# Kernel optimization log

Hardware: AMD Instinct MI355X
Metric: run time of the kernel (lower is better)

The kernel has to match this reference:

```python
import jax, jax.numpy as jnp
import numpy as np

U, I, E, D, R = 100000, 50000, 2000000, 64, 5


def setup_inputs() -> dict:
    key = jax.random.key(0)
    ks = jax.random.split(key, 14)
    def n(k, shape, scale=0.05):
        return jax.random.normal(k, shape, jnp.float32) * scale
    return {
        "user_feat": n(ks[0], (U, D), 1.0),
        "item_feat": n(ks[1], (I, D), 1.0),
        "rating_feat": n(ks[2], (R, D), 1.0),
        "row_idxs": jax.random.randint(ks[3], (E,), 0, I),   # item index per edge
        "col_idxs": jax.random.randint(ks[4], (E,), 0, U),   # user index per edge (dst)
        "rating": jax.random.randint(ks[5], (E,), 0, R),
        # gv = Linear(2D,D)+ReLU -> Linear(D,D)+ReLU
        "gv_w1": n(ks[6], (2 * D, D)), "gv_b1": jnp.zeros((D,), jnp.float32),
        "gv_w2": n(ks[7], (D, D)),     "gv_b2": jnp.zeros((D,), jnp.float32),
        # Attention: Linear(2D,D)+ReLU -> Linear(D,D)+ReLU -> Linear(D,1)
        "att_w1": n(ks[8], (2 * D, D)), "att_b1": jnp.zeros((D,), jnp.float32),
        "att_w2": n(ks[9], (D, D)),     "att_b2": jnp.zeros((D,), jnp.float32),
        "att_w3": n(ks[10], (D, 1)),    "att_b3": jnp.zeros((1,), jnp.float32),
        # output projection w = Linear(D,D)
        "w_w": n(ks[11], (D, D)), "w_b": jnp.zeros((D,), jnp.float32),
    }


def segment_softmax(logits, seg, num_segments):
    # numerically stable softmax over edges grouped by destination node
    m = jax.ops.segment_max(logits, seg, num_segments=num_segments)
    e = jnp.exp(logits - m[seg])
    s = jax.ops.segment_sum(e, seg, num_segments=num_segments)
    return e / s[seg]


def reference(user_feat, item_feat, rating_feat, row_idxs, col_idxs, rating,
              gv_w1, gv_b1, gv_w2, gv_b2,
              att_w1, att_b1, att_w2, att_b2, att_w3, att_b3,
              w_w, w_b):
    # gather per-edge embeddings
    r_emb = rating_feat[rating]          # [E, D]
    i_emb = item_feat[row_idxs]          # [E, D]
    u_emb = user_feat[col_idxs]          # [E, D]
    # gv MLP on concat(item, rating)
    x = jnp.concatenate([i_emb, r_emb], axis=1)              # [E, 2D]
    h1 = jax.nn.relu(x @ gv_w1 + gv_b1)
    x_ia = jax.nn.relu(h1 @ gv_w2 + gv_b2)                   # [E, D]
    # attention MLP on concat(x_ia, user)
    a = jnp.concatenate([x_ia, u_emb], axis=1)               # [E, 2D]
    a = jax.nn.relu(a @ att_w1 + att_b1)
    a = jax.nn.relu(a @ att_w2 + att_b2)
    weight = (a @ att_w3 + att_b3)[:, 0]                     # [E]
    # edge_softmax over incoming edges of each destination (user) node
    value = segment_softmax(weight, col_idxs, U)             # [E]
    # scatter-sum weighted messages to users
    h = jax.ops.segment_sum(x_ia * value[:, None], col_idxs, num_segments=U)  # [U, D]
    # act is None -> plain linear
    return h @ w_w + w_b
```

## Files before the change

kernel.cpp:

```cpp
#include <hip/hip_runtime.h>
#include <hip/hip_bf16.h>

#define U_N 100000
#define I_N 50000
#define E_N 2000000
#define R_N 5
#define C_N (I_N*R_N)
#define NBLK_U 391
#define NBLK_E 7813
#define NBLK_C 1954
#define NBUCKC 196

typedef __hip_bfloat16 bf16_t;
typedef unsigned short u16;
typedef unsigned char u8;
typedef __attribute__((ext_vector_type(8))) short bf16x8;
typedef __attribute__((ext_vector_type(4))) float f32x4;

__device__ __forceinline__ float blo(unsigned u){ return __uint_as_float(u<<16); }
__device__ __forceinline__ float bhi(unsigned u){ return __uint_as_float(u & 0xffff0000u); }
__device__ __forceinline__ unsigned pkbf(float a, float b){
  __hip_bfloat162 t = __float22bfloat162_rn(float2{a,b});
  union { __hip_bfloat162 h; unsigned u; } cv; cv.h = t; return cv.u;
}
__device__ __forceinline__ u16 f2b(float v){
  union { __hip_bfloat16 h; u16 u; } cv; cv.h = __float2bfloat16(v); return cv.u;
}
__device__ __forceinline__ unsigned relu_add_pk(unsigned a, unsigned b){
  return pkbf(fmaxf(blo(a)+blo(b),0.f), fmaxf(bhi(a)+bhi(b),0.f));
}

__global__ __launch_bounds__(256) void k_histQ(const int* __restrict__ cols, int* __restrict__ hist_g){
  __shared__ int histI[NBUCKC];
  int t = threadIdx.x, b = blockIdx.x;
  if(t < NBUCKC) histI[t] = 0;
  __syncthreads();
  int e = b*256 + t;
  if(e < E_N) atomicAdd(&histI[cols[e] >> 9], 1);
  __syncthreads();
  if(t < NBUCKC) hist_g[(size_t)b*NBUCKC + t] = histI[t];
}

__global__ __launch_bounds__(256) void k_scanQ(const int* __restrict__ hist_g, int* __restrict__ boff_g,
                                               int* __restrict__ qtot){
  __shared__ int wsum[4];
  int t = threadIdx.x, q = blockIdx.x;
  int lane = t & 63, wv = t >> 6;
  int running = 0;
  for(int c0=0; c0<NBLK_E; c0+=256){
    int b = c0 + t;
    int v = (b < NBLK_E) ? hist_g[(size_t)b*NBUCKC + q] : 0;
    int inc = v;
#pragma unroll
    for(int off=1; off<64; off<<=1){
      int x = __shfl(inc, lane-off);
      if(lane >= off) inc += x;
    }
    if(lane == 63) wsum[wv] = inc;
    __syncthreads();
    int w0=wsum[0], w1=wsum[1], w2=wsum[2], w3=wsum[3];
    int wpre = (wv>0?w0:0) + (wv>1?w1:0) + (wv>2?w2:0);
    if(b < NBLK_E) boff_g[(size_t)b*NBUCKC + q] = running + wpre + inc - v;
    running += w0 + w1 + w2 + w3;
    __syncthreads();
  }
  if(t == 0) qtot[q] = running;
}

__global__ void k_scanT(const int* __restrict__ qtot, int* __restrict__ qbase){
  __shared__ int s[256];
  int t = threadIdx.x;
  int v = (t < NBUCKC) ? qtot[t] : 0;
  s[t] = v; __syncthreads();
  for(int off=1; off<256; off<<=1){
    int x = (t>=off) ? s[t-off] : 0;
    __syncthreads();
    s[t] += x;
    __syncthreads();
  }
  if(t < NBUCKC) qbase[t] = s[t] - v;
  if(t == 255)   qbase[NBUCKC] = s[255];
}

__global__ __launch_bounds__(256) void k_place2(const int* __restrict__ rows, const int* __restrict__ cols,
                                                const int* __restrict__ rats,
                                                const int* __restrict__ boff_g, const int* __restrict__ qbase,
                                                unsigned* __restrict__ uc2){
  __shared__ int rankI[NBUCKC];
  __shared__ int baseI[NBUCKC];
  int t = threadIdx.x, b = blockIdx.x;
  if(t < NBUCKC){
    rankI[t] = 0;
    baseI[t] = qbase[t] + boff_g[(size_t)b*NBUCKC + t];
  }
  __syncthreads();
  int e = b*256 + t;
  if(e < E_N){
    int u = cols[e];
    int c = rows[e]*5 + rats[e];
    int q = u >> 9;
    int r = atomicAdd(&rankI[q], 1);
    uc2[baseI[q] + r] = ((unsigned)(u & 511) << 18) | (unsigned)c;
  }
}

__global__ __launch_bounds__(256) void k_fineB1(const unsigned* __restrict__ uc2, const int* __restrict__ qbase,
                                                int* __restrict__ cnt){
  __shared__ int hist[512];
  int t = threadIdx.x, q = blockIdx.x;
  hist[t] = 0; hist[t+256] = 0;
  __syncthreads();
  int r0 = qbase[q], r1 = qbase[q+1];
  for(int j=r0+t; j<r1; j+=256) atomicAdd(&hist[(uc2[j]>>18) & 511], 1);
  __syncthreads();
  cnt[q*512 + t]       = hist[t];
  cnt[q*512 + t + 256] = hist[t+256];
}

__global__ __launch_bounds__(256) void k_scanA(const int* __restrict__ cnt, int* __restrict__ start,
                                               int* __restrict__ bsum){
  __shared__ int s[256];
  int t = threadIdx.x, i = blockIdx.x*256 + t;
  int v = (i < U_N) ? cnt[i] : 0;
  s[t] = v; __syncthreads();
  for(int off=1; off<256; off<<=1){
    int x = (t>=off) ? s[t-off] : 0;
    __syncthreads();
    s[t] += x;
    __syncthreads();
  }
  start[i] = s[t] - v;
  if(t == 255) bsum[blockIdx.x] = s[255];
}

__global__ void k_scanB(int* bsum, int n){
  __shared__ int s[512];
  int t = threadIdx.x;
  int v = (t < n) ? bsum[t] : 0;
  s[t] = v; __syncthreads();
  for(int off=1; off<512; off<<=1){
    int x = (t>=off) ? s[t-off] : 0;
    __syncthreads();
    s[t] += x;
    __syncthreads();
  }
  if(t < n) bsum[t] = s[t] - v;
}

__global__ __launch_bounds__(256) void k_scanC(int* start, const int* __restrict__ bsum){
  int i = blockIdx.x*256 + threadIdx.x;
  start[i] += bsum[blockIdx.x];
}

__global__ __launch_bounds__(256) void k_fineB2(const unsigned* __restrict__ uc2, const int* __restrict__ qbase,
                                                const int* __restrict__ start,
                                                int* __restrict__ u_s, int* __restrict__ c_s){
  __shared__ int fillb[512];
  __shared__ int startb[512];
  int t = threadIdx.x, q = blockIdx.x;
  fillb[t] = 0; fillb[t+256] = 0;
  startb[t]     = start[q*512 + t];
  startb[t+256] = start[q*512 + t + 256];
  __syncthreads();
  int r0 = qbase[q], r1 = qbase[q+1];
  for(int j=r0+t; j<r1; j+=256){
    unsigned v = uc2[j];
    int ul = (int)((v>>18) & 511);
    int off = atomicAdd(&fillb[ul], 1);
    int pos = startb[ul] + off;
    u_s[pos] = (q<<9) | ul;
    c_s[pos] = (int)(v & 0x3FFFFu);
  }
}

__global__ void k_ratpart(const float* __restrict__ rf, const float* __restrict__ w1,
                          const float* __restrict__ b1, float* __restrict__ out){
  int t = threadIdx.x; if(t >= R_N*64) return;
  int r = t>>6, d = t&63;
  float acc = b1[d];
  for(int k=0;k<64;k++) acc += rf[r*64 + k] * w1[(64+k)*64 + d];
  out[t] = acc;
}

__global__ __launch_bounds__(256) void k_prepw6(const float* __restrict__ w1, const float* __restrict__ a1,
                                                const float* __restrict__ w2, const float* __restrict__ a2,
                                                const float* __restrict__ ww,
                                                u16* w1t, u16* u1t, u16* w2t, u16* a1t, u16* a2t, u16* wwt){
  int idx = (blockIdx.x & 15)*256 + threadIdx.x;
  int sec = blockIdx.x >> 4;
  int d = idx >> 6, k = idx & 63;
  const float* src; u16* dst; int ko = 0;
  switch(sec){
    case 0: src=w1; dst=w1t; break;
    case 1: src=a1; dst=u1t; ko=64; break;
    case 2: src=w2; dst=w2t; break;
    case 3: src=a1; dst=a1t; break;
    case 4: src=a2; dst=a2t; break;
    default: src=ww; dst=wwt; break;
  }
  dst[idx] = f2b(src[(size_t)(ko+k)*64 + d]);
}

template<bool BIAS>
__global__ __launch_bounds__(256) void k_rowgemm(const float4* __restrict__ in,
                                                 const uint4* __restrict__ wt,
                                                 const float* __restrict__ bias,
                                                 uint4* __restrict__ outp, int n){
  __shared__ uint4 A_u4[2048];
  __shared__ uint4 W_u4[512];
  __shared__ float bsh[64];
  u16* A16 = (u16*)A_u4;
  const int tid = threadIdx.x;
  for(int cid = tid; cid < 512; cid += 256){
    int dd = cid >> 3, ch = cid & 7;
    W_u4[dd*8 + (ch ^ (dd&7))] = wt[cid];
  }
  if(BIAS && tid < 64) bsh[tid] = bias[tid];
  const int base = blockIdx.x*256;
  const int ch = tid & 7;
#pragma unroll
  for(int it=0; it<8; ++it){
    int s = it*32 + (tid>>3);
    int r = base + s;
    uint4 o = {0,0,0,0};
    if(r < n){
      const float4* p = in + (size_t)r*16 + ch*2;
      float4 v0 = p[0], v1 = p[1];
      o.x = pkbf(v0.x, v0.y); o.y = pkbf(v0.z, v0.w);
      o.z = pkbf(v1.x, v1.y); o.w = pkbf(v1.z, v1.w);
    }
    A_u4[s*8 + (ch ^ (s&7))] = o;
  }
  __syncthreads();
  const int l = tid & 63, w = tid >> 6;
  const int lr = l & 15, g = l >> 4;
  bf16x8 bfr[4][2];
#pragma unroll
  for(int nt=0; nt<4; ++nt)
#pragma unroll
    for(int kk=0; kk<2; ++kk){
      int d = nt*16 + lr;
      bfr[nt][kk] = *(const bf16x8*)&W_u4[d*8 + ((kk*4+g) ^ (d&7))];
    }
  float bv[4];
#pragma unroll
  for(int nt=0; nt<4; ++nt) bv[nt] = BIAS ? bsh[nt*16 + lr] : 0.f;
#pragma unroll
  for(int t=0; t<4; ++t){
    int s = w*64 + t*16 + lr;
    bf16x8 af0 = *(const bf16x8*)&A_u4[s*8 + ((0*4+g) ^ (s&7))];
    bf16x8 af1 = *(const bf16x8*)&A_u4[s*8 + ((1*4+g) ^ (s&7))];
    f32x4 acc[4];
#pragma unroll
    for(int nt=0; nt<4; ++nt){
      f32x4 c0 = { bv[nt], bv[nt], bv[nt], bv[nt] };
      c0 = __builtin_amdgcn_mfma_f32_16x16x32_bf16(af0, bfr[nt][0], c0, 0, 0, 0);
      c0 = __builtin_amdgcn_mfma_f32_16x16x32_bf16(af1, bfr[nt][1], c0, 0, 0, 0);
      acc[nt] = c0;
    }
#pragma unroll
    for(int nt=0; nt<4; ++nt){
      int d = nt*16 + lr;
#pragma unroll
      for(int reg=0; reg<4; ++reg){
        int srow = w*64 + t*16 + g*4 + reg;
        A16[srow*64 + ((d>>3)^(srow&7))*8 + (d&7)] = f2b(acc[nt][reg]);
      }
    }
  }
#pragma unroll
  for(int it=0; it<8; ++it){
    int s = w*64 + it*8 + (l>>3);
    int c2 = l & 7;
    int r = base + s;
    if(r < n) outp[(size_t)r*8 + c2] = A_u4[s*8 + (c2 ^ (s&7))];
  }
}

__global__ __launch_bounds__(256) void k_combo_mfma(const uint4* __restrict__ itemp,
                                                    const float4* __restrict__ ratp,
                                                    const uint4* __restrict__ w2t_g, const uint4* __restrict__ a1t_g,
                                                    const uint4* __restrict__ wwt_g,
                                                    const float* __restrict__ b2,
                                                    uint4* __restrict__ y_o, uint4* __restrict__ xa1_o){
  __shared__ uint4 A_u4[1024];
  __shared__ uint4 X_u4[1024];
  __shared__ uint4 W2_u4[512];
  __shared__ uint4 A1_u4[512];
  __shared__ uint4 WW_u4[512];
  __shared__ float4 rsh4[80];
  __shared__ float b2sh[64];
  u16* A16 = (u16*)A_u4;
  u16* X16 = (u16*)X_u4;
  const int tid = threadIdx.x;
  for(int cid = tid; cid < 512; cid += 256){
    int dd = cid >> 3, ch = cid & 7;
    W2_u4[dd*8 + (ch ^ (dd&7))] = w2t_g[cid];
    A1_u4[dd*8 + (ch ^ (dd&7))] = a1t_g[cid];
    WW_u4[dd*8 + (ch ^ (dd&7))] = wwt_g[cid];
  }
  if(tid < 80) rsh4[tid] = ratp[tid];
  if(tid < 64) b2sh[tid] = b2[tid];
  __syncthreads();

  const int base = blockIdx.x*128;
  const int ch = tid & 7;
#pragma unroll
  for(int it=0; it<4; ++it){
    int s = it*32 + (tid>>3);
    int cidx = base + s;
    uint4 o = {0,0,0,0};
    if(cidx < C_N){
      int i = cidx/5, r = cidx - i*5;
      uint4 iv = itemp[(size_t)i*8 + ch];
      float4 r0 = rsh4[r*16 + ch*2], r1 = rsh4[r*16 + ch*2 + 1];
      o.x = pkbf(fmaxf(blo(iv.x)+r0.x,0.f), fmaxf(bhi(iv.x)+r0.y,0.f));
      o.y = pkbf(fmaxf(blo(iv.y)+r0.z,0.f), fmaxf(bhi(iv.y)+r0.w,0.f));
      o.z = pkbf(fmaxf(blo(iv.z)+r1.x,0.f), fmaxf(bhi(iv.z)+r1.y,0.f));
      o.w = pkbf(fmaxf(blo(iv.w)+r1.z,0.f), fmaxf(bhi(iv.w)+r1.w,0.f));
    }
    A_u4[s*8 + (ch ^ (s&7))] = o;
  }
  __syncthreads();

  const int l = tid & 63, w = tid >> 6;
  const int lr = l & 15, g = l >> 4;
  bf16x8 w2f[4][2], a1f[4][2], wwf[4][2];
#pragma unroll
  for(int nt=0; nt<4; ++nt)
#pragma unroll
    for(int kk=0; kk<2; ++kk){
      int d = nt*16 + lr;
      w2f[nt][kk] = *(const bf16x8*)&W2_u4[d*8 + ((kk*4+g) ^ (d&7))];
      a1f[nt][kk] = *(const bf16x8*)&A1_u4[d*8 + ((kk*4+g) ^ (d&7))];
      wwf[nt][kk] = *(const bf16x8*)&WW_u4[d*8 + ((kk*4+g) ^ (d&7))];
    }
  float b2v[4];
#pragma unroll
  for(int nt=0; nt<4; ++nt) b2v[nt] = b2sh[nt*16 + lr];

#pragma unroll
  for(int t=0; t<2; ++t){
    int s = w*32 + t*16 + lr;
    bf16x8 af0 = *(const bf16x8*)&A_u4[s*8 + ((0*4+g) ^ (s&7))];
    bf16x8 af1 = *(const bf16x8*)&A_u4[s*8 + ((1*4+g) ^ (s&7))];
#pragma unroll
    for(int nt=0; nt<4; ++nt){
      f32x4 c0 = { b2v[nt], b2v[nt], b2v[nt], b2v[nt] };
      c0 = __builtin_amdgcn_mfma_f32_16x16x32_bf16(af0, w2f[nt][0], c0, 0, 0, 0);
      c0 = __builtin_amdgcn_mfma_f32_16x16x32_bf16(af1, w2f[nt][1], c0, 0, 0, 0);
      int d = nt*16 + lr;
#pragma unroll
      for(int reg=0; reg<4; ++reg){
        int srow = w*32 + t*16 + g*4 + reg;
        X16[srow*64 + ((d>>3)^(srow&7))*8 + (d&7)] = f2b(fmaxf(c0[reg], 0.f));
      }
    }
    bf16x8 xf0 = *(const bf16x8*)&X_u4[s*8 + ((0*4+g) ^ (s&7))];
    bf16x8 xf1 = *(const bf16x8*)&X_u4[s*8 + ((1*4+g) ^ (s&7))];
#pragma unroll
    for(int nt=0; nt<4; ++nt){
      f32x4 c0 = { 0.f, 0.f, 0.f, 0.f };
      c0 = __builtin_amdgcn_mfma_f32_16x16x32_bf16(xf0, a1f[nt][0], c0, 0, 0, 0);
      c0 = __builtin_amdgcn_mfma_f32_16x16x32_bf16(xf1, a1f[nt][1], c0, 0, 0, 0);
      int d = nt*16 + lr;
#pragma unroll
      for(int reg=0; reg<4; ++reg){
        int srow = w*32 + t*16 + g*4 + reg;
        A16[srow*64 + ((d>>3)^(srow&7))*8 + (d&7)] = f2b(c0[reg]);
      }
    }
#pragma unroll
    for(int nt=0; nt<4; ++nt){
      f32x4 c0 = { 0.f, 0.f, 0.f, 0.f };
      c0 = __builtin_amdgcn_mfma_f32_16x16x32_bf16(xf0, wwf[nt][0], c0, 0, 0, 0);
      c0 = __builtin_amdgcn_mfma_f32_16x16x32_bf16(xf1, wwf[nt][1], c0, 0, 0, 0);
      int d = nt*16 + lr;
#pragma unroll
      for(int reg=0; reg<4; ++reg){
        int srow = w*32 + t*16 + g*4 + reg;
        X16[srow*64 + ((d>>3)^(srow&7))*8 + (d&7)] = f2b(c0[reg]);
      }
    }
  }
#pragma unroll
  for(int it=0; it<4; ++it){
    int s = w*32 + it*8 + (l>>3);
    int c2 = l & 7;
    int r = base + s;
    if(r < C_N){
      y_o  [(size_t)r*8 + c2] = X_u4[s*8 + (c2 ^ (s&7))];
      xa1_o[(size_t)r*8 + c2] = A_u4[s*8 + (c2 ^ (s&7))];
    }
  }
}

__global__ __launch_bounds__(256) void k_edge_mfma(const int* __restrict__ u_s, const int* __restrict__ c_s,
                                                   const uint4* __restrict__ xa1p, const uint4* __restrict__ userp,
                                                   const u16* __restrict__ w2t_g,
                                                   const float* __restrict__ a2b,
                                                   const float* __restrict__ a3w, const float* __restrict__ a3b,
                                                   float* __restrict__ wlog){
  const int tid = threadIdx.x;
  const int base = blockIdx.x*256;
  const int l = tid & 63, w = tid >> 6;
  const int lr = l & 15;
  const int g  = l >> 4;
  bf16x8 bf[4][2];
#pragma unroll
  for(int nt=0; nt<4; ++nt)
#pragma unroll
    for(int kk=0; kk<2; ++kk){
      int d = nt*16 + lr;
      bf[nt][kk] = *(const bf16x8*)(w2t_g + d*64 + kk*32 + g*8);
    }
  float b2v[4], a3v[4];
#pragma unroll
  for(int nt=0; nt<4; ++nt){ b2v[nt] = a2b[nt*16 + lr]; a3v[nt] = a3w[nt*16 + lr]; }
  const float a3b0 = a3b[0];

  int cin[4], uin[4];
#pragma unroll
  for(int t=0; t<4; ++t){
    int s = base + w*64 + t*16 + lr;
    cin[t] = (s < E_N) ? c_s[s] : 0;
    uin[t] = (s < E_N) ? u_s[s] : 0;
  }
  uint4 xv0 = xa1p[(size_t)cin[0]*8 + g];
  uint4 uv0 = userp[(size_t)uin[0]*8 + g];
  uint4 xv1 = xa1p[(size_t)cin[0]*8 + 4 + g];
  uint4 uv1 = userp[(size_t)uin[0]*8 + 4 + g];

#pragma unroll
  for(int t=0; t<4; ++t){
    uint4 nx0, nu0, nx1, nu1;
    if(t < 3){
      nx0 = xa1p[(size_t)cin[t+1]*8 + g];
      nu0 = userp[(size_t)uin[t+1]*8 + g];
      nx1 = xa1p[(size_t)cin[t+1]*8 + 4 + g];
      nu1 = userp[(size_t)uin[t+1]*8 + 4 + g];
    }
    union { uint4 u4; bf16x8 v; } a0, a1;
    a0.u4.x = relu_add_pk(xv0.x, uv0.x);
    a0.u4.y = relu_add_pk(xv0.y, uv0.y);
    a0.u4.z = relu_add_pk(xv0.z, uv0.z);
    a0.u4.w = relu_add_pk(xv0.w, uv0.w);
    a1.u4.x = relu_add_pk(xv1.x, uv1.x);
    a1.u4.y = relu_add_pk(xv1.y, uv1.y);
    a1.u4.z = relu_add_pk(xv1.z, uv1.z);
    a1.u4.w = relu_add_pk(xv1.w, uv1.w);
    f32x4 acc[4];
#pragma unroll
    for(int nt=0; nt<4; ++nt){
      f32x4 c0 = { b2v[nt], b2v[nt], b2v[nt], b2v[nt] };
      c0 = __builtin_amdgcn_mfma_f32_16x16x32_bf16(a0.v, bf[nt][0], c0, 0, 0, 0);
      c0 = __builtin_amdgcn_mfma_f32_16x16x32_bf16(a1.v, bf[nt][1], c0, 0, 0, 0);
      acc[nt] = c0;
    }
    float s0=0.f, s1=0.f, s2=0.f, s3=0.f;
#pragma unroll
    for(int nt=0; nt<4; ++nt){
      s0 += fmaxf(acc[nt][0], 0.f) * a3v[nt];
      s1 += fmaxf(acc[nt][1], 0.f) * a3v[nt];
      s2 += fmaxf(acc[nt][2], 0.f) * a3v[nt];
      s3 += fmaxf(acc[nt][3], 0.f) * a3v[nt];
    }
#pragma unroll
    for(int mask=1; mask<16; mask<<=1){
      s0 += __shfl_xor(s0, mask);
      s1 += __shfl_xor(s1, mask);
      s2 += __shfl_xor(s2, mask);
      s3 += __shfl_xor(s3, mask);
    }
    if(lr == 0){
      int e0 = base + w*64 + t*16 + g*4;
      if(e0+0 < E_N) wlog[e0+0] = s0 + a3b0;
      if(e0+1 < E_N) wlog[e0+1] = s1 + a3b0;
      if(e0+2 < E_N) wlog[e0+2] = s2 + a3b0;
      if(e0+3 < E_N) wlog[e0+3] = s3 + a3b0;
    }
    xv0 = nx0; uv0 = nu0; xv1 = nx1; uv1 = nu1;
  }
}

__global__ __launch_bounds__(256) void k_smax(const int* __restrict__ start,
                                              const float* __restrict__ wlog,
                                              u16* __restrict__ pval){
  int w = threadIdx.x >> 6, lane = threadIdx.x & 63;
  int u = blockIdx.x*4 + w;
  int s0 = start[u], n = start[u+1] - s0;
  int nq = (n + 63) >> 6;
  float tq[4];
  float m = -1e30f;
  for(int q=0; q<nq; ++q){
    int j = q*64 + lane;
    float t = (j<n) ? wlog[s0+j] : -1e30f;
    if(q<4) tq[q] = t;
    m = fmaxf(m, t);
  }
#pragma unroll
  for(int off=32; off>=1; off>>=1) m = fmaxf(m, __shfl_xor(m, off));
  float ssum = 0.f;
  for(int q=0; q<nq; ++q){
    int j = q*64 + lane;
    float t = (q<4) ? tq[q] : ((j<n) ? wlog[s0+j] : -1e30f);
    float e = (j<n) ? __expf(t - m) : 0.f;
    if(q<4) tq[q] = e;
    ssum += e;
  }
#pragma unroll
  for(int off=32; off>=1; off>>=1) ssum += __shfl_xor(ssum, off);
  float inv = (n>0) ? (1.f/ssum) : 0.f;
  for(int q=0; q<nq; ++q){
    int j = q*64 + lane;
    float e = (q<4) ? tq[q] : ((j<n) ? __expf(wlog[s0+j] - m) : 0.f);
    if(j<n) pval[s0+j] = f2b(e * inv);
  }
}

__global__ __launch_bounds__(256) void k_agg(const int* __restrict__ start,
                                             const int* __restrict__ u_s, const int* __restrict__ c_s,
                                             const u16* __restrict__ pval,
                                             const u16* __restrict__ Y,
                                             const float* __restrict__ wb,
                                             float* __restrict__ out){
  __shared__ uint4 Ysh[4][256];
  int w = threadIdx.x >> 6, l = threadIdx.x & 63;
  int lr = l & 15, g = l >> 4;
  int base = (blockIdx.x*4 + w) * 16;
  if(base >= U_N) return;
  int s0g = start[base];
  int s1g = start[base+16];
  int myu = base + lr;
  float wbv[4];
#pragma unroll
  for(int nt=0; nt<4; ++nt) wbv[nt] = wb[nt*16 + lr];
  f32x4 acc[4];
#pragma unroll
  for(int nt=0; nt<4; ++nt) acc[nt] = f32x4{ wbv[nt], wbv[nt], wbv[nt], wbv[nt] };

  u16* Ysh16 = (u16*)&Ysh[w][0];
  const int kb = g*8;
  int sA = s0g & ~31;
  int nch = (s1g - sA + 31) >> 5;
  for(int ch=0; ch<nch; ++ch){
    int e0 = sA + ch*32;
    int rowe = e0 + (l>>1);
    int crow = c_s[rowe];
    const uint4* yp = (const uint4*)Y + (size_t)crow*8 + (l&1)*4;
    uint4* dst = &Ysh[w][(l>>1)*8 + (l&1)*4];
    dst[0] = yp[0]; dst[1] = yp[1]; dst[2] = yp[2]; dst[3] = yp[3];

    bf16x8 pv = *(const bf16x8*)(pval + e0 + kb);
    int4 u0 = *(const int4*)(u_s + e0 + kb);
    int4 u1 = *(const int4*)(u_s + e0 + kb + 4);
    bf16x8 af;
    af[0] = (u0.x == myu) ? pv[0] : (short)0;
    af[1] = (u0.y == myu) ? pv[1] : (short)0;
    af[2] = (u0.z == myu) ? pv[2] : (short)0;
    af[3] = (u0.w == myu) ? pv[3] : (short)0;
    af[4] = (u1.x == myu) ? pv[4] : (short)0;
    af[5] = (u1.y == myu) ? pv[5] : (short)0;
    af[6] = (u1.z == myu) ? pv[6] : (short)0;
    af[7] = (u1.w == myu) ? pv[7] : (short)0;
    bf16x8 b0, b1, b2, b3;
#pragma unroll
    for(int j=0; j<8; ++j){
      int r = (kb + j)*64 + lr;
      b0[j] = (short)Ysh16[r];
      b1[j] = (short)Ysh16[r+16];
      b2[j] = (short)Ysh16[r+32];
      b3[j] = (short)Ysh16[r+48];
    }
    acc[0] = __builtin_amdgcn_mfma_f32_16x16x32_bf16(af, b0, acc[0], 0, 0, 0);
    acc[1] = __builtin_amdgcn_mfma_f32_16x16x32_bf16(af, b1, acc[1], 0, 0, 0);
    acc[2] = __builtin_amdgcn_mfma_f32_16x16x32_bf16(af, b2, acc[2], 0, 0, 0);
    acc[3] = __builtin_amdgcn_mfma_f32_16x16x32_bf16(af, b3, acc[3], 0, 0, 0);
  }
#pragma unroll
  for(int nt=0; nt<4; ++nt){
#pragma unroll
    for(int reg=0; reg<4; ++reg){
      int u = base + g*4 + reg;
      out[(size_t)u*64 + nt*16 + lr] = acc[nt][reg];
    }
  }
}

extern "C" void kernel_launch(void* const* d_in, const int* in_sizes, int n_in,
                              void* d_out, int out_size, void* d_ws, size_t ws_size,
                              hipStream_t stream){
  (void)in_sizes; (void)n_in; (void)out_size; (void)ws_size;
  const float4* user_feat  = (const float4*)d_in[0];
  const float4* item_feat  = (const float4*)d_in[1];
  const float*  rating_feat= (const float*)d_in[2];
  const int*    rows       = (const int*)d_in[3];
  const int*    cols       = (const int*)d_in[4];
  const int*    rats       = (const int*)d_in[5];
  const float* gv_w1 = (const float*)d_in[6];
  const float* gv_b1 = (const float*)d_in[7];
  const float* gv_w2 = (const float*)d_in[8];
  const float* gv_b2 = (const float*)d_in[9];
  const float* att_w1= (const float*)d_in[10];
  const float* att_b1= (const float*)d_in[11];
  const float* att_w2= (const float*)d_in[12];
  const float* att_b2= (const float*)d_in[13];
  const float* att_w3= (const float*)d_in[14];
  const float* att_b3= (const float*)d_in[15];
  const float* w_w   = (const float*)d_in[16];
  const float* w_b   = (const float*)d_in[17];
  float* out = (float*)d_out;

  char* ws = (char*)d_ws; size_t off = 0;
  auto take = [&](size_t b)->char*{ char* p = ws + off; off = (off + b + 255) & ~(size_t)255; return p; };
  bf16_t*   item_part  = (bf16_t*)take((size_t)I_N*64*2);
  bf16_t*   user_part  = (bf16_t*)take((size_t)U_N*64*2);
  float*    rating_part= (float*) take((size_t)R_N*64*4);
  bf16_t*   y_t        = (bf16_t*)take((size_t)C_N*64*2);
  bf16_t*   xa1_t      = (bf16_t*)take((size_t)C_N*64*2);
  float*    wlog_s     = (float*) take((size_t)E_N*4);
  int*      c_s        = (int*)   take((size_t)E_N*4);
  int*      u_s        = (int*)   take((size_t)E_N*4);
  u16*      pval       = (u16*)   take((size_t)E_N*2);
  unsigned* uc2        = (unsigned*)take((size_t)E_N*4);
  int*      hist_g     = (int*)   take((size_t)NBLK_E*NBUCKC*4);
  int*      boff_g     = (int*)   take((size_t)NBLK_E*NBUCKC*4);
  int*      qtot       = (int*)   take((size_t)256*4);
  int*      qbase      = (int*)   take((size_t)256*4);
  int*      cnt        = (int*)   take((size_t)(NBUCKC*512+256)*4);
  int*      start      = (int*)   take((size_t)(NBUCKC*512+256)*4);
  int*      bsum       = (int*)   take((size_t)512*4);
  u16*      w1t        = (u16*)   take((size_t)4096*2);
  u16*      u1t        = (u16*)   take((size_t)4096*2);
  u16*      w2t        = (u16*)   take((size_t)4096*2);
  u16*      a1t        = (u16*)   take((size_t)4096*2);
  u16*      a2t        = (u16*)   take((size_t)4096*2);
  u16*      wwt        = (u16*)   take((size_t)4096*2);

  k_histQ <<<NBLK_E, 256, 0, stream>>>(cols, hist_g);
  k_scanQ <<<NBUCKC, 256, 0, stream>>>(hist_g, boff_g, qtot);
  k_scanT <<<1, 256, 0, stream>>>(qtot, qbase);
  k_place2<<<NBLK_E, 256, 0, stream>>>(rows, cols, rats, boff_g, qbase, uc2);
  k_fineB1<<<NBUCKC, 256, 0, stream>>>(uc2, qbase, cnt);
  k_scanA <<<NBLK_U, 256, 0, stream>>>(cnt, start, bsum);
  k_scanB <<<1, 512, 0, stream>>>(bsum, NBLK_U);
  k_scanC <<<NBLK_U, 256, 0, stream>>>(start, bsum);
  k_fineB2<<<NBUCKC, 256, 0, stream>>>(uc2, qbase, start, u_s, c_s);
  k_ratpart <<<1, 320, 0, stream>>>(rating_feat, gv_w1, gv_b1, rating_part);
  k_prepw6  <<<96, 256, 0, stream>>>(gv_w1, att_w1, gv_w2, att_w2, w_w, w1t, u1t, w2t, a1t, a2t, wwt);
  k_rowgemm<false><<<(I_N+255)/256, 256, 0, stream>>>(item_feat, (const uint4*)w1t, nullptr,
                                                      (uint4*)item_part, I_N);
  k_rowgemm<true> <<<NBLK_U, 256, 0, stream>>>(user_feat, (const uint4*)u1t, att_b1,
                                               (uint4*)user_part, U_N);
  k_combo_mfma<<<NBLK_C, 256, 0, stream>>>((const uint4*)item_part, (const float4*)rating_part,
                                           (const uint4*)w2t, (const uint4*)a1t, (const uint4*)wwt, gv_b2,
                                           (uint4*)y_t, (uint4*)xa1_t);
  k_edge_mfma<<<NBLK_E, 256, 0, stream>>>(u_s, c_s, (const uint4*)xa1_t, (const uint4*)user_part,
                                          w2t, att_b2, att_w3, att_b3, wlog_s);
  k_smax <<<U_N/4, 256, 0, stream>>>(start, wlog_s, pval);
  k_agg  <<<(U_N/64)+1, 256, 0, stream>>>(start, u_s, c_s, pval, (const u16*)y_t, w_b, out);
}
```

Measured before the change: 329.5 us.

## Store xa1 table in FP8 and fuse segment softmax into aggregation kernel

The per-(item,rating) attention pre-activation table is now written as FP8 e4m3 instead of bf16, which halves the bytes each edge gathers in the edge MLP kernel. The separate softmax kernel and its bf16 probability array are removed. The aggregation kernel now computes the per-user max in a first pass over the edges, then exponentiates inside the MFMA accumulation loop and normalizes by the sum at the end. This saves a kernel launch and a round trip of per-edge values, but reads the logits and user ids twice and loses precision from the FP8 storage.

```diff
diff --git a/kernel.cpp b/kernel.cpp
--- a/kernel.cpp
+++ b/kernel.cpp
@@ -1,5 +1,6 @@
 #include <hip/hip_runtime.h>
 #include <hip/hip_bf16.h>
+#include <hip/hip_fp8.h>
 
 #define U_N 100000
 #define I_N 50000
@@ -26,8 +27,11 @@
 __device__ __forceinline__ u16 f2b(float v){
   union { __hip_bfloat16 h; u16 u; } cv; cv.h = __float2bfloat16(v); return cv.u;
 }
-__device__ __forceinline__ unsigned relu_add_pk(unsigned a, unsigned b){
-  return pkbf(fmaxf(blo(a)+blo(b),0.f), fmaxf(bhi(a)+bhi(b),0.f));
+__device__ __forceinline__ float f8f(unsigned b){
+  __hip_fp8_e4m3 h; h.__x = (u8)b; return (float)h;
+}
+__device__ __forceinline__ unsigned ff8(float f){
+  __hip_fp8_e4m3 h(f); return (unsigned)h.__x;
 }
 
 __global__ __launch_bounds__(256) void k_histQ(const int* __restrict__ cols, int* __restrict__ hist_g){
@@ -282,7 +286,7 @@
                                                     const uint4* __restrict__ w2t_g, const uint4* __restrict__ a1t_g,
                                                     const uint4* __restrict__ wwt_g,
                                                     const float* __restrict__ b2,
-                                                    uint4* __restrict__ y_o, uint4* __restrict__ xa1_o){
+                                                    uint4* __restrict__ y_o, u8* __restrict__ xa1_o8){
   __shared__ uint4 A_u4[1024];
   __shared__ uint4 X_u4[1024];
   __shared__ uint4 W2_u4[512];
@@ -388,15 +392,30 @@
     int s = w*32 + it*8 + (l>>3);
     int c2 = l & 7;
     int r = base + s;
+    if(r < C_N) y_o[(size_t)r*8 + c2] = X_u4[s*8 + (c2 ^ (s&7))];
+  }
+#pragma unroll
+  for(int it=0; it<2; ++it){
+    int slot = it*64 + l;
+    int rl = slot >> 2;
+    int c4 = slot & 3;
+    int s = w*32 + rl;
+    int r = base + s;
     if(r < C_N){
-      y_o  [(size_t)r*8 + c2] = X_u4[s*8 + (c2 ^ (s&7))];
-      xa1_o[(size_t)r*8 + c2] = A_u4[s*8 + (c2 ^ (s&7))];
+      uint4 h0 = A_u4[s*8 + ((c4*2+0) ^ (s&7))];
+      uint4 h1 = A_u4[s*8 + ((c4*2+1) ^ (s&7))];
+      uint4 o;
+      o.x = ff8(blo(h0.x)) | (ff8(bhi(h0.x))<<8) | (ff8(blo(h0.y))<<16) | (ff8(bhi(h0.y))<<24);
+      o.y = ff8(blo(h0.z)) | (ff8(bhi(h0.z))<<8) | (ff8(blo(h0.w))<<16) | (ff8(bhi(h0.w))<<24);
+      o.z = ff8(blo(h1.x)) | (ff8(bhi(h1.x))<<8) | (ff8(blo(h1.y))<<16) | (ff8(bhi(h1.y))<<24);
+      o.w = ff8(blo(h1.z)) | (ff8(bhi(h1.z))<<8) | (ff8(blo(h1.w))<<16) | (ff8(bhi(h1.w))<<24);
+      *(uint4*)(xa1_o8 + (size_t)r*64 + c4*16) = o;
     }
   }
 }
 
 __global__ __launch_bounds__(256) void k_edge_mfma(const int* __restrict__ u_s, const int* __restrict__ c_s,
-                                                   const uint4* __restrict__ xa1p, const uint4* __restrict__ userp,
+                                                   const u8* __restrict__ xa1p8, const uint4* __restrict__ userp,
                                                    const u16* __restrict__ w2t_g,
                                                    const float* __restrict__ a2b,
                                                    const float* __restrict__ a3w, const float* __restrict__ a3b,
@@ -426,29 +445,29 @@
     cin[t] = (s < E_N) ? c_s[s] : 0;
     uin[t] = (s < E_N) ? u_s[s] : 0;
   }
-  uint4 xv0 = xa1p[(size_t)cin[0]*8 + g];
+  uint2 xq0 = *(const uint2*)(xa1p8 + (size_t)cin[0]*64 + g*8);
+  uint2 xq1 = *(const uint2*)(xa1p8 + (size_t)cin[0]*64 + 32 + g*8);
   uint4 uv0 = userp[(size_t)uin[0]*8 + g];
-  uint4 xv1 = xa1p[(size_t)cin[0]*8 + 4 + g];
   uint4 uv1 = userp[(size_t)uin[0]*8 + 4 + g];
 
 #pragma unroll
   for(int t=0; t<4; ++t){
-    uint4 nx0, nu0, nx1, nu1;
+    uint2 nx0, nx1; uint4 nu0, nu1;
     if(t < 3){
-      nx0 = xa1p[(size_t)cin[t+1]*8 + g];
+      nx0 = *(const uint2*)(xa1p8 + (size_t)cin[t+1]*64 + g*8);
+      nx1 = *(const uint2*)(xa1p8 + (size_t)cin[t+1]*64 + 32 + g*8);
       nu0 = userp[(size_t)uin[t+1]*8 + g];
-      nx1 = xa1p[(size_t)cin[t+1]*8 + 4 + g];
       nu1 = userp[(size_t)uin[t+1]*8 + 4 + g];
     }
     union { uint4 u4; bf16x8 v; } a0, a1;
-    a0.u4.x = relu_add_pk(xv0.x, uv0.x);
-    a0.u4.y = relu_add_pk(xv0.y, uv0.y);
-    a0.u4.z = relu_add_pk(xv0.z, uv0.z);
-    a0.u4.w = relu_add_pk(xv0.w, uv0.w);
-    a1.u4.x = relu_add_pk(xv1.x, uv1.x);
-    a1.u4.y = relu_add_pk(xv1.y, uv1.y);
-    a1.u4.z = relu_add_pk(xv1.z, uv1.z);
-    a1.u4.w = relu_add_pk(xv1.w, uv1.w);
+    a0.u4.x = pkbf(fmaxf(f8f(xq0.x&255u)+blo(uv0.x),0.f),       fmaxf(f8f((xq0.x>>8)&255u)+bhi(uv0.x),0.f));
+    a0.u4.y = pkbf(fmaxf(f8f((xq0.x>>16)&255u)+blo(uv0.y),0.f), fmaxf(f8f(xq0.x>>24)+bhi(uv0.y),0.f));
+    a0.u4.z = pkbf(fmaxf(f8f(xq0.y&255u)+blo(uv0.z),0.f),       fmaxf(f8f((xq0.y>>8)&255u)+bhi(uv0.z),0.f));
+    a0.u4.w = pkbf(fmaxf(f8f((xq0.y>>16)&255u)+blo(uv0.w),0.f), fmaxf(f8f(xq0.y>>24)+bhi(uv0.w),0.f));
+    a1.u4.x = pkbf(fmaxf(f8f(xq1.x&255u)+blo(uv1.x),0.f),       fmaxf(f8f((xq1.x>>8)&255u)+bhi(uv1.x),0.f));
+    a1.u4.y = pkbf(fmaxf(f8f((xq1.x>>16)&255u)+blo(uv1.y),0.f), fmaxf(f8f(xq1.x>>24)+bhi(uv1.y),0.f));
+    a1.u4.z = pkbf(fmaxf(f8f(xq1.y&255u)+blo(uv1.z),0.f),       fmaxf(f8f((xq1.y>>8)&255u)+bhi(uv1.z),0.f));
+    a1.u4.w = pkbf(fmaxf(f8f((xq1.y>>16)&255u)+blo(uv1.w),0.f), fmaxf(f8f(xq1.y>>24)+bhi(uv1.w),0.f));
     f32x4 acc[4];
 #pragma unroll
     for(int nt=0; nt<4; ++nt){
@@ -479,51 +498,16 @@
       if(e0+2 < E_N) wlog[e0+2] = s2 + a3b0;
       if(e0+3 < E_N) wlog[e0+3] = s3 + a3b0;
     }
-    xv0 = nx0; uv0 = nu0; xv1 = nx1; uv1 = nu1;
-  }
-}
-
-__global__ __launch_bounds__(256) void k_smax(const int* __restrict__ start,
+    xq0 = nx0; xq1 = nx1; uv0 = nu0; uv1 = nu1;
+  }
+}
+
+__global__ __launch_bounds__(256) void k_aggf(const int* __restrict__ start,
+                                              const int* __restrict__ u_s, const int* __restrict__ c_s,
                                               const float* __restrict__ wlog,
-                                              u16* __restrict__ pval){
-  int w = threadIdx.x >> 6, lane = threadIdx.x & 63;
-  int u = blockIdx.x*4 + w;
-  int s0 = start[u], n = start[u+1] - s0;
-  int nq = (n + 63) >> 6;
-  float tq[4];
-  float m = -1e30f;
-  for(int q=0; q<nq; ++q){
-    int j = q*64 + lane;
-    float t = (j<n) ? wlog[s0+j] : -1e30f;
-    if(q<4) tq[q] = t;
-    m = fmaxf(m, t);
-  }
-#pragma unroll
-  for(int off=32; off>=1; off>>=1) m = fmaxf(m, __shfl_xor(m, off));
-  float ssum = 0.f;
-  for(int q=0; q<nq; ++q){
-    int j = q*64 + lane;
-    float t = (q<4) ? tq[q] : ((j<n) ? wlog[s0+j] : -1e30f);
-    float e = (j<n) ? __expf(t - m) : 0.f;
-    if(q<4) tq[q] = e;
-    ssum += e;
-  }
-#pragma unroll
-  for(int off=32; off>=1; off>>=1) ssum += __shfl_xor(ssum, off);
-  float inv = (n>0) ? (1.f/ssum) : 0.f;
-  for(int q=0; q<nq; ++q){
-    int j = q*64 + lane;
-    float e = (q<4) ? tq[q] : ((j<n) ? __expf(wlog[s0+j] - m) : 0.f);
-    if(j<n) pval[s0+j] = f2b(e * inv);
-  }
-}
-
-__global__ __launch_bounds__(256) void k_agg(const int* __restrict__ start,
-                                             const int* __restrict__ u_s, const int* __restrict__ c_s,
-                                             const u16* __restrict__ pval,
-                                             const u16* __restrict__ Y,
-                                             const float* __restrict__ wb,
-                                             float* __restrict__ out){
+                                              const u16* __restrict__ Y,
+                                              const float* __restrict__ wb,
+                                              float* __restrict__ out){
   __shared__ uint4 Ysh[4][256];
   int w = threadIdx.x >> 6, l = threadIdx.x & 63;
   int lr = l & 15, g = l >> 4;
@@ -532,17 +516,34 @@
   int s0g = start[base];
   int s1g = start[base+16];
   int myu = base + lr;
-  float wbv[4];
-#pragma unroll
-  for(int nt=0; nt<4; ++nt) wbv[nt] = wb[nt*16 + lr];
-  f32x4 acc[4];
-#pragma unroll
-  for(int nt=0; nt<4; ++nt) acc[nt] = f32x4{ wbv[nt], wbv[nt], wbv[nt], wbv[nt] };
-
-  u16* Ysh16 = (u16*)&Ysh[w][0];
-  const int kb = g*8;
   int sA = s0g & ~31;
   int nch = (s1g - sA + 31) >> 5;
+  const int kb = g*8;
+
+  float m = -1e30f;
+  for(int ch=0; ch<nch; ++ch){
+    int e0 = sA + ch*32;
+    float4 wv0 = *(const float4*)(wlog + e0 + kb);
+    float4 wv1 = *(const float4*)(wlog + e0 + kb + 4);
+    int4 u0 = *(const int4*)(u_s + e0 + kb);
+    int4 u1 = *(const int4*)(u_s + e0 + kb + 4);
+    if(u0.x==myu) m = fmaxf(m, wv0.x);
+    if(u0.y==myu) m = fmaxf(m, wv0.y);
+    if(u0.z==myu) m = fmaxf(m, wv0.z);
+    if(u0.w==myu) m = fmaxf(m, wv0.w);
+    if(u1.x==myu) m = fmaxf(m, wv1.x);
+    if(u1.y==myu) m = fmaxf(m, wv1.y);
+    if(u1.z==myu) m = fmaxf(m, wv1.z);
+    if(u1.w==myu) m = fmaxf(m, wv1.w);
+  }
+  m = fmaxf(m, __shfl_xor(m, 16));
+  m = fmaxf(m, __shfl_xor(m, 32));
+
+  f32x4 acc[4];
+#pragma unroll
+  for(int nt=0; nt<4; ++nt) acc[nt] = f32x4{0.f,0.f,0.f,0.f};
+  float ssum = 0.f;
+  u16* Ysh16 = (u16*)&Ysh[w][0];
   for(int ch=0; ch<nch; ++ch){
     int e0 = sA + ch*32;
     int rowe = e0 + (l>>1);
@@ -551,18 +552,22 @@
     uint4* dst = &Ysh[w][(l>>1)*8 + (l&1)*4];
     dst[0] = yp[0]; dst[1] = yp[1]; dst[2] = yp[2]; dst[3] = yp[3];
 
-    bf16x8 pv = *(const bf16x8*)(pval + e0 + kb);
+    float4 wv0 = *(const float4*)(wlog + e0 + kb);
+    float4 wv1 = *(const float4*)(wlog + e0 + kb + 4);
     int4 u0 = *(const int4*)(u_s + e0 + kb);
     int4 u1 = *(const int4*)(u_s + e0 + kb + 4);
     bf16x8 af;
-    af[0] = (u0.x == myu) ? pv[0] : (short)0;
-    af[1] = (u0.y == myu) ? pv[1] : (short)0;
-    af[2] = (u0.z == myu) ? pv[2] : (short)0;
-    af[3] = (u0.w == myu) ? pv[3] : (short)0;
-    af[4] = (u1.x == myu) ? pv[4] : (short)0;
-    af[5] = (u1.y == myu) ? pv[5] : (short)0;
-    af[6] = (u1.z == myu) ? pv[6] : (short)0;
-    af[7] = (u1.w == myu) ? pv[7] : (short)0;
+    {
+      bool mt; float e;
+      mt = (u0.x==myu); e = __expf((mt?wv0.x:-1e30f) - m); ssum += mt?e:0.f; af[0] = mt?(short)f2b(e):(short)0;
+      mt = (u0.y==myu); e = __expf((mt?wv0.y:-1e30f) - m); ssum += mt?e:0.f; af[1] = mt?(short)f2b(e):(short)0;
+      mt = (u0.z==myu); e = __expf((mt?wv0.z:-1e30f) - m); ssum += mt?e:0.f; af[2] = mt?(short)f2b(e):(short)0;
+      mt = (u0.w==myu); e = __expf((mt?wv0.w:-1e30f) - m); ssum += mt?e:0.f; af[3] = mt?(short)f2b(e):(short)0;
+      mt = (u1.x==myu); e = __expf((mt?wv1.x:-1e30f) - m); ssum += mt?e:0.f; af[4] = mt?(short)f2b(e):(short)0;
+      mt = (u1.y==myu); e = __expf((mt?wv1.y:-1e30f) - m); ssum += mt?e:0.f; af[5] = mt?(short)f2b(e):(short)0;
+      mt = (u1.z==myu); e = __expf((mt?wv1.z:-1e30f) - m); ssum += mt?e:0.f; af[6] = mt?(short)f2b(e):(short)0;
+      mt = (u1.w==myu); e = __expf((mt?wv1.w:-1e30f) - m); ssum += mt?e:0.f; af[7] = mt?(short)f2b(e):(short)0;
+    }
     bf16x8 b0, b1, b2, b3;
 #pragma unroll
     for(int j=0; j<8; ++j){
@@ -577,13 +582,19 @@
     acc[2] = __builtin_amdgcn_mfma_f32_16x16x32_bf16(af, b2, acc[2], 0, 0, 0);
     acc[3] = __builtin_amdgcn_mfma_f32_16x16x32_bf16(af, b3, acc[3], 0, 0, 0);
   }
-#pragma unroll
-  for(int nt=0; nt<4; ++nt){
-#pragma unroll
-    for(int reg=0; reg<4; ++reg){
-      int u = base + g*4 + reg;
-      out[(size_t)u*64 + nt*16 + lr] = acc[nt][reg];
-    }
+  ssum += __shfl_xor(ssum, 16);
+  ssum += __shfl_xor(ssum, 32);
+  float inv = (ssum > 0.f) ? (1.f/ssum) : 0.f;
+  float wbv[4];
+#pragma unroll
+  for(int nt=0; nt<4; ++nt) wbv[nt] = wb[nt*16 + lr];
+#pragma unroll
+  for(int reg=0; reg<4; ++reg){
+    float sc = __shfl(inv, g*4 + reg);
+    int u = base + g*4 + reg;
+#pragma unroll
+    for(int nt=0; nt<4; ++nt)
+      out[(size_t)u*64 + nt*16 + lr] = acc[nt][reg]*sc + wbv[nt];
   }
 }
 
@@ -617,11 +628,10 @@
   bf16_t*   user_part  = (bf16_t*)take((size_t)U_N*64*2);
   float*    rating_part= (float*) take((size_t)R_N*64*4);
   bf16_t*   y_t        = (bf16_t*)take((size_t)C_N*64*2);
-  bf16_t*   xa1_t      = (bf16_t*)take((size_t)C_N*64*2);
+  u8*       xa1_8      = (u8*)    take((size_t)C_N*64);
   float*    wlog_s     = (float*) take((size_t)E_N*4);
   int*      c_s        = (int*)   take((size_t)E_N*4);
   int*      u_s        = (int*)   take((size_t)E_N*4);
-  u16*      pval       = (u16*)   take((size_t)E_N*2);
   unsigned* uc2        = (unsigned*)take((size_t)E_N*4);
   int*      hist_g     = (int*)   take((size_t)NBLK_E*NBUCKC*4);
   int*      boff_g     = (int*)   take((size_t)NBLK_E*NBUCKC*4);
@@ -654,9 +664,8 @@
                                                (uint4*)user_part, U_N);
   k_combo_mfma<<<NBLK_C, 256, 0, stream>>>((const uint4*)item_part, (const float4*)rating_part,
                                            (const uint4*)w2t, (const uint4*)a1t, (const uint4*)wwt, gv_b2,
-                                           (uint4*)y_t, (uint4*)xa1_t);
-  k_edge_mfma<<<NBLK_E, 256, 0, stream>>>(u_s, c_s, (const uint4*)xa1_t, (const uint4*)user_part,
+                                           (uint4*)y_t, xa1_8);
+  k_edge_mfma<<<NBLK_E, 256, 0, stream>>>(u_s, c_s, xa1_8, (const uint4*)user_part,
                                           w2t, att_b2, att_w3, att_b3, wlog_s);
-  k_smax <<<U_N/4, 256, 0, stream>>>(start, wlog_s, pval);
-  k_agg  <<<(U_N/64)+1, 256, 0, stream>>>(start, u_s, c_s, pval, (const u16*)y_t, w_b, out);
-}
+  k_aggf <<<(U_N/64)+1, 256, 0, stream>>>(start, u_s, c_s, wlog_s, (const u16*)y_t, w_b, out);
+}
```

New measurement: 310.5 us. -5.8%, faster.
